# Kernel optimization log

Measured on AMD Instinct MI355X. Metric: run time of the kernel, lower is better.

Reference implementation:

```python
import jax, jax.numpy as jnp
import numpy as np

N = 50000      # nodes
E = 800000     # edges (avg degree 16)
DIN = 128
HID = 128
OUT = 10       # classes
G = 64         # graphs in batch


def setup_inputs() -> dict:
    key = jax.random.key(0)
    ks = jax.random.split(key, 10)
    x = jax.random.normal(ks[0], (N, DIN), dtype=jnp.float32)
    edge_index = jax.random.randint(ks[1], (2, E), 0, N, dtype=jnp.int32)
    edge_weight = jax.random.uniform(ks[2], (E,), dtype=jnp.float32)
    batch = jnp.sort(jax.random.randint(ks[3], (N,), 0, G, dtype=jnp.int32))
    W1 = jax.random.normal(ks[4], (DIN, HID), dtype=jnp.float32) / np.sqrt(DIN)
    b1 = jnp.zeros((HID,), dtype=jnp.float32)
    W2 = jax.random.normal(ks[5], (HID, HID), dtype=jnp.float32) / np.sqrt(HID)
    b2 = jnp.zeros((HID,), dtype=jnp.float32)
    W3 = jax.random.normal(ks[6], (HID, OUT), dtype=jnp.float32) / np.sqrt(HID)
    b3 = jnp.zeros((OUT,), dtype=jnp.float32)
    return {"x": x, "edge_index": edge_index, "edge_weight": edge_weight,
            "batch": batch, "W1": W1, "b1": b1, "W2": W2, "b2": b2,
            "W3": W3, "b3": b3}


def _gcn_norm(edge_index, edge_weight, n_nodes):
    # PyG gcn_norm: add self-loops with weight 1, D^-1/2 (A+I) D^-1/2
    loop = jnp.arange(n_nodes, dtype=edge_index.dtype)
    src = jnp.concatenate([edge_index[0], loop])
    dst = jnp.concatenate([edge_index[1], loop])
    w = jnp.concatenate([edge_weight, jnp.ones((n_nodes,), edge_weight.dtype)])
    deg = jax.ops.segment_sum(w, dst, num_segments=n_nodes)
    dinv = jnp.where(deg > 0, jax.lax.rsqrt(deg), 0.0)
    norm = dinv[src] * w * dinv[dst]
    return src, dst, norm


def _gcn_conv(x, W, b, src, dst, norm, n_nodes):
    h = x @ W                                      # [N, F] dense transform
    msg = norm[:, None] * h[src]                   # gather + scale  [E+N, F]
    out = jax.ops.segment_sum(msg, dst, num_segments=n_nodes)  # scatter-add
    return out + b


def reference(x, edge_index, edge_weight, batch, W1, b1, W2, b2, W3, b3):
    src, dst, norm = _gcn_norm(edge_index, edge_weight, N)
    h = jax.nn.relu(_gcn_conv(x, W1, b1, src, dst, norm, N))
    h = jax.nn.relu(_gcn_conv(h, W2, b2, src, dst, norm, N))
    h = _gcn_conv(h, W3, b3, src, dst, norm, N)    # [N, OUT]
    # global_mean_pool over graph ids
    sums = jax.ops.segment_sum(h, batch, num_segments=G)          # [G, OUT]
    cnts = jax.ops.segment_sum(jnp.ones((N,), h.dtype), batch, num_segments=G)
    pooled = sums / jnp.maximum(cnts, 1.0)[:, None]
    return jax.nn.log_softmax(pooled, axis=1)
```

## Files before the change

kernel.cpp:

```cpp
#include <hip/hip_runtime.h>
#include <math.h>

#define NN 50000
#define EE 800000
#define GG 64
#define FD 128
#define OUTD 10
#define NB 49

typedef __attribute__((ext_vector_type(8))) short s8v;
typedef __attribute__((ext_vector_type(4))) float f4v;

static __device__ inline unsigned short f2b(float f) {
    unsigned int u = __float_as_uint(f);
    return (unsigned short)((u + 0x7FFFu + ((u >> 16) & 1u)) >> 16);
}

#define DEG_SCALE 4294967296.0
#define DEG_MASK  ((1ull << 44) - 1)


__global__ void k_prep(unsigned long long* packed, const float* __restrict__ W1,
                       const float* __restrict__ W2, unsigned short* __restrict__ Wt1,
                       unsigned short* __restrict__ Wt2, int n) {
    int i = blockIdx.x * blockDim.x + threadIdx.x;
    if (i < n) packed[i] = (1ull << 44) | (1ull << 32);
    if (i < FD * FD) {
        int nn = i >> 7, k = i & 127;
        Wt1[i] = f2b(W1[k * FD + nn]);
        Wt2[i] = f2b(W2[k * FD + nn]);
    }
}

__global__ void k_degree(const int* __restrict__ dst, const float* __restrict__ w,
                         unsigned long long* packed, unsigned* __restrict__ rank, int e) {
    int i = blockIdx.x * blockDim.x + threadIdx.x;
    if (i >= e) return;
    unsigned long long q = (unsigned long long)((double)w[i] * DEG_SCALE + 0.5);
    unsigned long long old = atomicAdd(&packed[dst[i]], (1ull << 44) | q);
    rank[i] = (unsigned)(old >> 44) - 1u;
}

__global__ __launch_bounds__(1024) void k_scanA(const unsigned long long* __restrict__ packed,
        int* __restrict__ rowptr, int* __restrict__ blocksum,
        float* __restrict__ dinv, int n) {
    __shared__ int wtot[16];
    int tid = threadIdx.x;
    int i = blockIdx.x * 1024 + tid;
    int lane = tid & 63, wv = tid >> 6;
    int v = 0;
    if (i < n) {
        unsigned long long p = packed[i];
        v = (int)(p >> 44);
        float deg = (float)((double)(p & DEG_MASK) * (1.0 / DEG_SCALE));
        dinv[i] = 1.0f / sqrtf(deg);
    }
    int s = v;
    #pragma unroll
    for (int off = 1; off < 64; off <<= 1) {
        int u = __shfl_up(s, off, 64);
        if (lane >= off) s += u;
    }
    if (lane == 63) wtot[wv] = s;
    __syncthreads();
    int wpre = 0;
    for (int j = 0; j < wv; ++j) wpre += wtot[j];
    if (i < n) rowptr[i] = wpre + s - v;
    if (tid == 1023) blocksum[blockIdx.x] = wpre + s;
}

__global__ void k_scanB(int* blocksum, int* rowptr) {
    int l = threadIdx.x;
    int v = (l < NB) ? blocksum[l] : 0;
    int s = v;
    #pragma unroll
    for (int off = 1; off < 64; off <<= 1) {
        int u = __shfl_up(s, off, 64);
        if (l >= off) s += u;
    }
    if (l < NB) blocksum[l] = s - v;
    if (l == NB - 1) rowptr[NN] = s;
}

__global__ __launch_bounds__(1024) void k_scanC(int* __restrict__ rowptr,
        const int* __restrict__ blocksum, const unsigned long long* __restrict__ packed,
        const float* __restrict__ dinv, uint2* __restrict__ ent, int n) {
    int i = blockIdx.x * 1024 + threadIdx.x;
    if (i >= n) return;
    int r = rowptr[i] + blocksum[blockIdx.x];
    rowptr[i] = r;
    int cnt = (int)(packed[i] >> 44);
    float di = dinv[i];
    ent[r + cnt - 1] = make_uint2((unsigned)i, __float_as_uint(di * di));
}

__global__ void k_fill(const int* __restrict__ src, const int* __restrict__ dst,
                       const float* __restrict__ w, const float* __restrict__ dinv,
                       const int* __restrict__ rowptr, const unsigned* __restrict__ rank,
                       uint2* __restrict__ ent, int e) {
    int i = blockIdx.x * blockDim.x + threadIdx.x;
    if (i >= e) return;
    int s = src[i], d = dst[i];
    int pos = rowptr[d] + (int)rank[i];
    float v = dinv[s] * w[i] * dinv[d];
    ent[pos] = make_uint2((unsigned)s, __float_as_uint(v));
}

__global__ void k_bounds(const int* __restrict__ batch, int* __restrict__ gstart, int n) {
    int i = blockIdx.x * blockDim.x + threadIdx.x;
    if (i >= n) return;
    int b = batch[i];
    int bp = (i == 0) ? -1 : batch[i - 1];
    for (int g = bp + 1; g <= b; ++g) gstart[g] = i;
    if (i == n - 1)
        for (int g = b + 1; g <= GG; ++g) gstart[g] = n;
}

__global__ __launch_bounds__(256) void k_gemm_f32in(const float* __restrict__ A,
        const unsigned short* __restrict__ Wt, unsigned short* __restrict__ out, int n) {
    int tid = threadIdx.x;
    int wave = tid >> 6, lane = tid & 63;
    int quad = lane >> 4, c16 = lane & 15;
    int rowbase = blockIdx.x * 64 + wave * 16;
    int rowA = rowbase + c16;
    if (rowA >= n) rowA = n - 1;
    f4v acc[8];
    #pragma unroll
    for (int t = 0; t < 8; ++t) acc[t] = (f4v){0.f, 0.f, 0.f, 0.f};

    #pragma unroll
    for (int k0 = 0; k0 < 128; k0 += 32) {
        const float* ap = A + (size_t)rowA * FD + k0 + quad * 8;
        float4 a0 = *(const float4*)ap;
        float4 a1 = *(const float4*)(ap + 4);
        s8v a;
        a[0] = (short)f2b(a0.x); a[1] = (short)f2b(a0.y);
        a[2] = (short)f2b(a0.z); a[3] = (short)f2b(a0.w);
        a[4] = (short)f2b(a1.x); a[5] = (short)f2b(a1.y);
        a[6] = (short)f2b(a1.z); a[7] = (short)f2b(a1.w);
        #pragma unroll
        for (int t = 0; t < 8; ++t) {
            s8v b = *(const s8v*)(Wt + (size_t)(t * 16 + c16) * FD + k0 + quad * 8);
            acc[t] = __builtin_amdgcn_mfma_f32_16x16x32_bf16(a, b, acc[t], 0, 0, 0);
        }
    }
    #pragma unroll
    for (int t = 0; t < 8; ++t) {
        #pragma unroll
        for (int r = 0; r < 4; ++r) {
            int row = rowbase + quad * 4 + r;
            if (row < n) out[(size_t)row * FD + t * 16 + c16] = f2b(acc[t][r]);
        }
    }
}

__global__ __launch_bounds__(256) void k_gemm_bf(const unsigned short* __restrict__ A,
        const unsigned short* __restrict__ Wt, unsigned short* __restrict__ out, int n) {
    int tid = threadIdx.x;
    int wave = tid >> 6, lane = tid & 63;
    int quad = lane >> 4, c16 = lane & 15;
    int rowbase = blockIdx.x * 64 + wave * 16;
    int rowA = rowbase + c16;
    if (rowA >= n) rowA = n - 1;
    f4v acc[8];
    #pragma unroll
    for (int t = 0; t < 8; ++t) acc[t] = (f4v){0.f, 0.f, 0.f, 0.f};

    #pragma unroll
    for (int k0 = 0; k0 < 128; k0 += 32) {
        s8v a = *(const s8v*)(A + (size_t)rowA * FD + k0 + quad * 8);
        #pragma unroll
        for (int t = 0; t < 8; ++t) {
            s8v b = *(const s8v*)(Wt + (size_t)(t * 16 + c16) * FD + k0 + quad * 8);
            acc[t] = __builtin_amdgcn_mfma_f32_16x16x32_bf16(a, b, acc[t], 0, 0, 0);
        }
    }
    #pragma unroll
    for (int t = 0; t < 8; ++t) {
        #pragma unroll
        for (int r = 0; r < 4; ++r) {
            int row = rowbase + quad * 4 + r;
            if (row < n) out[(size_t)row * FD + t * 16 + c16] = f2b(acc[t][r]);
        }
    }
}

__global__ void k_gemm10(const unsigned short* __restrict__ A, const float* __restrict__ W,
                         float* __restrict__ out, int n) {
    __shared__ float Ws[FD * OUTD];
    int tid = threadIdx.x;
    for (int i = tid; i < FD * OUTD; i += blockDim.x) Ws[i] = W[i];
    __syncthreads();
    int i = blockIdx.x * blockDim.x + tid;
    if (i >= n) return;
    float acc[OUTD];
    #pragma unroll
    for (int c = 0; c < OUTD; ++c) acc[c] = 0.0f;
    const unsigned short* a = A + (size_t)i * FD;
    for (int k0 = 0; k0 < FD; k0 += 8) {
        uint4 t = *(const uint4*)(a + k0);
        float av[8];
        av[0] = __uint_as_float(t.x << 16); av[1] = __uint_as_float(t.x & 0xFFFF0000u);
        av[2] = __uint_as_float(t.y << 16); av[3] = __uint_as_float(t.y & 0xFFFF0000u);
        av[4] = __uint_as_float(t.z << 16); av[5] = __uint_as_float(t.z & 0xFFFF0000u);
        av[6] = __uint_as_float(t.w << 16); av[7] = __uint_as_float(t.w & 0xFFFF0000u);
        #pragma unroll
        for (int j = 0; j < 8; ++j)
            #pragma unroll
            for (int c = 0; c < OUTD; ++c) acc[c] += av[j] * Ws[(k0 + j) * OUTD + c];
    }
    float* o = out + (size_t)i * OUTD;
    #pragma unroll
    for (int c = 0; c < OUTD; ++c) o[c] = acc[c];
}

__global__ __launch_bounds__(256) void k_spmm_bf(const int* __restrict__ rowptr,
        const uint2* __restrict__ ent, const unsigned short* __restrict__ tin,
        const float* __restrict__ bias, unsigned short* __restrict__ out,
        int n, int dorelu) {
    int w = (blockIdx.x * blockDim.x + threadIdx.x) >> 6;
    int lane = threadIdx.x & 63;
    if (w >= n) return;
    int c = lane & 15, g = lane >> 4;
    int beg = rowptr[w], end = rowptr[w + 1];
    float acc[8];
    #pragma unroll
    for (int j = 0; j < 8; ++j) acc[j] = 0.0f;
    for (int e0 = beg; e0 < end; e0 += 16) {
        uint2 en[4];
        uint4 t[4];
        #pragma unroll
        for (int u = 0; u < 4; ++u) {
            int e = e0 + 4 * u + g;
            en[u] = (e < end) ? ent[e] : make_uint2(0u, 0u);
        }
        #pragma unroll
        for (int u = 0; u < 4; ++u)
            t[u] = *(const uint4*)(tin + (size_t)en[u].x * FD + c * 8);
        #pragma unroll
        for (int u = 0; u < 4; ++u) {
            float v = __uint_as_float(en[u].y);
            acc[0] += v * __uint_as_float(t[u].x << 16);
            acc[1] += v * __uint_as_float(t[u].x & 0xFFFF0000u);
            acc[2] += v * __uint_as_float(t[u].y << 16);
            acc[3] += v * __uint_as_float(t[u].y & 0xFFFF0000u);
            acc[4] += v * __uint_as_float(t[u].z << 16);
            acc[5] += v * __uint_as_float(t[u].z & 0xFFFF0000u);
            acc[6] += v * __uint_as_float(t[u].w << 16);
            acc[7] += v * __uint_as_float(t[u].w & 0xFFFF0000u);
        }
    }
    #pragma unroll
    for (int j = 0; j < 8; ++j) {
        acc[j] += __shfl_xor(acc[j], 16, 64);
        acc[j] += __shfl_xor(acc[j], 32, 64);
    }
    if (g == 0) {
        uint4 r;
        float o[8];
        #pragma unroll
        for (int j = 0; j < 8; ++j) {
            float x = acc[j] + bias[c * 8 + j];
            o[j] = dorelu ? fmaxf(x, 0.0f) : x;
        }
        r.x = (unsigned)f2b(o[0]) | ((unsigned)f2b(o[1]) << 16);
        r.y = (unsigned)f2b(o[2]) | ((unsigned)f2b(o[3]) << 16);
        r.z = (unsigned)f2b(o[4]) | ((unsigned)f2b(o[5]) << 16);
        r.w = (unsigned)f2b(o[6]) | ((unsigned)f2b(o[7]) << 16);
        *(uint4*)(out + (size_t)w * FD + c * 8) = r;
    }
}

__global__ void k_spmm10(const int* __restrict__ rowptr, const uint2* __restrict__ ent,
        const float* __restrict__ tin, const float* __restrict__ bias,
        float* __restrict__ out, int n) {
    int t = blockIdx.x * blockDim.x + threadIdx.x;
    int node = t / OUTD;
    int c = t - node * OUTD;
    if (node >= n) return;
    int beg = rowptr[node], end = rowptr[node + 1];
    float acc = 0.0f;
    for (int e = beg; e < end; ++e) {
        uint2 en = ent[e];
        acc += __uint_as_float(en.y) * tin[(size_t)en.x * OUTD + c];
    }
    out[(size_t)node * OUTD + c] = acc + bias[c];
}


__global__ __launch_bounds__(256) void k_poolfin(const float* __restrict__ h,
        const int* __restrict__ gstart, float* __restrict__ out) {
    int g = blockIdx.x;
    int beg = gstart[g], end = gstart[g + 1];
    int tid = threadIdx.x;
    int lane = tid & 63, wv = tid >> 6;
    float acc[OUTD];
    #pragma unroll
    for (int c = 0; c < OUTD; ++c) acc[c] = 0.0f;
    for (int i = beg + tid; i < end; i += 256) {
        const float* hp = h + (size_t)i * OUTD;
        #pragma unroll
        for (int c = 0; c < OUTD; ++c) acc[c] += hp[c];
    }
    #pragma unroll
    for (int off = 32; off >= 1; off >>= 1)
        #pragma unroll
        for (int c = 0; c < OUTD; ++c) acc[c] += __shfl_down(acc[c], off, 64);
    __shared__ float ws[4][OUTD];
    if (lane == 0)
        #pragma unroll
        for (int c = 0; c < OUTD; ++c) ws[wv][c] = acc[c];
    __syncthreads();
    if (tid == 0) {
        float cf = fmaxf((float)(end - beg), 1.0f);
        float v[OUTD], m = -1e30f;
        #pragma unroll
        for (int c = 0; c < OUTD; ++c) {
            v[c] = (ws[0][c] + ws[1][c] + ws[2][c] + ws[3][c]) / cf;
            m = fmaxf(m, v[c]);
        }
        float s = 0.0f;
        #pragma unroll
        for (int c = 0; c < OUTD; ++c) s += expf(v[c] - m);
        float l = logf(s);
        #pragma unroll
        for (int c = 0; c < OUTD; ++c) out[g * OUTD + c] = v[c] - m - l;
    }
}


extern "C" void kernel_launch(void* const* d_in, const int* in_sizes, int n_in,
                              void* d_out, int out_size, void* d_ws, size_t ws_size,
                              hipStream_t stream) {
    const float* x   = (const float*)d_in[0];
    const int*   ei  = (const int*)d_in[1];
    const float* ew  = (const float*)d_in[2];
    const int*   bat = (const int*)d_in[3];
    const float* W1  = (const float*)d_in[4];
    const float* b1  = (const float*)d_in[5];
    const float* W2  = (const float*)d_in[6];
    const float* b2  = (const float*)d_in[7];
    const float* W3  = (const float*)d_in[8];
    const float* b3  = (const float*)d_in[9];
    float* out = (float*)d_out;

    const int* src = ei;
    const int* dst = ei + EE;

    char* p = (char*)d_ws;
    auto alloc = [&](size_t bytes) -> void* {
        void* r = (void*)p;
        p += (bytes + 255) & ~(size_t)255;
        return r;
    };
    unsigned long long* packed = (unsigned long long*)alloc((size_t)NN * 8);
    float*          dinv   = (float*)alloc((size_t)NN * 4);
    int*            rowptr = (int*)  alloc((size_t)(NN + 1) * 4);
    unsigned*       rank   = (unsigned*)alloc((size_t)EE * 4);
    uint2*          ent    = (uint2*)alloc((size_t)(EE + NN) * 8);
    unsigned short* Wt1    = (unsigned short*)alloc((size_t)FD * FD * 2);
    unsigned short* Wt2    = (unsigned short*)alloc((size_t)FD * FD * 2);
    unsigned short* hA     = (unsigned short*)alloc((size_t)NN * FD * 2);
    unsigned short* hB     = (unsigned short*)alloc((size_t)NN * FD * 2);
    float*          bufC   = (float*)alloc((size_t)NN * OUTD * 4);
    float*          bufD   = (float*)alloc((size_t)NN * OUTD * 4);
    int*            bsum   = (int*)  alloc((size_t)(NB + 1) * 4);
    int*            gstart = (int*)  alloc((size_t)(GG + 1) * 4);
    (void)ws_size; (void)in_sizes; (void)n_in; (void)out_size;

    const int B = 256;
    k_prep  <<<(NN + B - 1) / B, B, 0, stream>>>(packed, W1, W2, Wt1, Wt2, NN);
    k_degree<<<(EE + B - 1) / B, B, 0, stream>>>(dst, ew, packed, rank, EE);
    k_scanA <<<NB, 1024, 0, stream>>>(packed, rowptr, bsum, dinv, NN);
    k_scanB <<<1, 64, 0, stream>>>(bsum, rowptr);
    k_scanC <<<NB, 1024, 0, stream>>>(rowptr, bsum, packed, dinv, ent, NN);
    k_fill  <<<(EE + B - 1) / B, B, 0, stream>>>(src, dst, ew, dinv, rowptr, rank, ent, EE);
    k_bounds<<<(NN + B - 1) / B, B, 0, stream>>>(bat, gstart, NN);

    k_gemm_f32in<<<(NN + 63) / 64, B, 0, stream>>>(x, Wt1, hA, NN);
    k_spmm_bf   <<<(NN * 64 + B - 1) / B, B, 0, stream>>>(rowptr, ent, hA, b1, hB, NN, 1);
    k_gemm_bf   <<<(NN + 63) / 64, B, 0, stream>>>(hB, Wt2, hA, NN);
    k_spmm_bf   <<<(NN * 64 + B - 1) / B, B, 0, stream>>>(rowptr, ent, hA, b2, hB, NN, 1);
    k_gemm10    <<<(NN + B - 1) / B, B, 0, stream>>>(hB, W3, bufC, NN);
    k_spmm10    <<<(NN * OUTD + B - 1) / B, B, 0, stream>>>(rowptr, ent, bufC, b3, bufD, NN);
    k_poolfin   <<<GG, 256, 0, stream>>>(bufD, gstart, out);
}
```

Baseline: 297.3 us.

## Merge preprocessing kernels and use single-pass decoupled scan

Fuses the first GEMM, the degree/rank atomics and the graph-bound computation into one heterogeneous launch partitioned by block index, so independent work shares one grid. Replaces the three-kernel scan (scanA/scanB/scanC) with a single kernel where each block publishes its sum and spins on flags of earlier blocks to get its base offset. This removes several launches and inter-kernel gaps. It relies on all 49 scan blocks being co-resident for the spin-wait to be safe.

```diff
diff --git a/kernel.cpp b/kernel.cpp
--- a/kernel.cpp
+++ b/kernel.cpp
@@ -7,6 +7,9 @@
 #define FD 128
 #define OUTD 10
 #define NB 49
+#define GB 782
+#define DB 3125
+#define BB 196
 
 typedef __attribute__((ext_vector_type(8))) short s8v;
 typedef __attribute__((ext_vector_type(4))) float f4v;
@@ -22,7 +25,7 @@
 
 __global__ void k_prep(unsigned long long* packed, const float* __restrict__ W1,
                        const float* __restrict__ W2, unsigned short* __restrict__ Wt1,
-                       unsigned short* __restrict__ Wt2, int n) {
+                       unsigned short* __restrict__ Wt2, int* __restrict__ bflag, int n) {
     int i = blockIdx.x * blockDim.x + threadIdx.x;
     if (i < n) packed[i] = (1ull << 44) | (1ull << 32);
     if (i < FD * FD) {
@@ -30,30 +33,93 @@
         Wt1[i] = f2b(W1[k * FD + nn]);
         Wt2[i] = f2b(W2[k * FD + nn]);
     }
-}
-
-__global__ void k_degree(const int* __restrict__ dst, const float* __restrict__ w,
-                         unsigned long long* packed, unsigned* __restrict__ rank, int e) {
-    int i = blockIdx.x * blockDim.x + threadIdx.x;
-    if (i >= e) return;
-    unsigned long long q = (unsigned long long)((double)w[i] * DEG_SCALE + 0.5);
-    unsigned long long old = atomicAdd(&packed[dst[i]], (1ull << 44) | q);
-    rank[i] = (unsigned)(old >> 44) - 1u;
-}
-
-__global__ __launch_bounds__(1024) void k_scanA(const unsigned long long* __restrict__ packed,
-        int* __restrict__ rowptr, int* __restrict__ blocksum,
-        float* __restrict__ dinv, int n) {
+    if (i < NB) bflag[i] = 0;
+}
+
+
+static __device__ inline void gemm_f32in_body(int bid, const float* __restrict__ A,
+        const unsigned short* __restrict__ Wt, unsigned short* __restrict__ out, int n) {
+    int tid = threadIdx.x;
+    int wave = tid >> 6, lane = tid & 63;
+    int quad = lane >> 4, c16 = lane & 15;
+    int rowbase = bid * 64 + wave * 16;
+    int rowA = rowbase + c16;
+    if (rowA >= n) rowA = n - 1;
+    f4v acc[8];
+    #pragma unroll
+    for (int t = 0; t < 8; ++t) acc[t] = (f4v){0.f, 0.f, 0.f, 0.f};
+    #pragma unroll
+    for (int k0 = 0; k0 < 128; k0 += 32) {
+        const float* ap = A + (size_t)rowA * FD + k0 + quad * 8;
+        float4 a0 = *(const float4*)ap;
+        float4 a1 = *(const float4*)(ap + 4);
+        s8v a;
+        a[0] = (short)f2b(a0.x); a[1] = (short)f2b(a0.y);
+        a[2] = (short)f2b(a0.z); a[3] = (short)f2b(a0.w);
+        a[4] = (short)f2b(a1.x); a[5] = (short)f2b(a1.y);
+        a[6] = (short)f2b(a1.z); a[7] = (short)f2b(a1.w);
+        #pragma unroll
+        for (int t = 0; t < 8; ++t) {
+            s8v b = *(const s8v*)(Wt + (size_t)(t * 16 + c16) * FD + k0 + quad * 8);
+            acc[t] = __builtin_amdgcn_mfma_f32_16x16x32_bf16(a, b, acc[t], 0, 0, 0);
+        }
+    }
+    #pragma unroll
+    for (int t = 0; t < 8; ++t) {
+        #pragma unroll
+        for (int r = 0; r < 4; ++r) {
+            int row = rowbase + quad * 4 + r;
+            if (row < n) out[(size_t)row * FD + t * 16 + c16] = f2b(acc[t][r]);
+        }
+    }
+}
+
+__global__ __launch_bounds__(256) void k_mega1(const float* __restrict__ x,
+        const unsigned short* __restrict__ Wt1, unsigned short* __restrict__ hA,
+        const int* __restrict__ dst, const float* __restrict__ ew,
+        unsigned long long* packed, unsigned* __restrict__ rank,
+        const int* __restrict__ batch, int* __restrict__ gstart) {
+    int b = blockIdx.x;
+    if (b < GB) {
+        gemm_f32in_body(b, x, Wt1, hA, NN);
+    } else if (b < GB + DB) {
+        int i = (b - GB) * 256 + threadIdx.x;
+        if (i < EE) {
+            unsigned long long q = (unsigned long long)((double)ew[i] * DEG_SCALE + 0.5);
+            unsigned long long old = atomicAdd(&packed[dst[i]], (1ull << 44) | q);
+            rank[i] = (unsigned)(old >> 44) - 1u;
+        }
+    } else {
+        int i = (b - GB - DB) * 256 + threadIdx.x;
+        if (i < NN) {
+            int bb = batch[i];
+            int bp = (i == 0) ? -1 : batch[i - 1];
+            for (int g = bp + 1; g <= bb; ++g) gstart[g] = i;
+            if (i == NN - 1)
+                for (int g = bb + 1; g <= GG; ++g) gstart[g] = NN;
+        }
+    }
+}
+
+
+__global__ __launch_bounds__(1024) void k_scan(const unsigned long long* __restrict__ packed,
+        int* __restrict__ rowptr, float* __restrict__ dinv, uint2* __restrict__ ent,
+        int* __restrict__ bsum, int* __restrict__ bflag, int n) {
     __shared__ int wtot[16];
+    __shared__ int sbase_sh;
     int tid = threadIdx.x;
-    int i = blockIdx.x * 1024 + tid;
+    int bid = blockIdx.x;
+    int i = bid * 1024 + tid;
     int lane = tid & 63, wv = tid >> 6;
+
     int v = 0;
+    float di = 0.0f;
     if (i < n) {
         unsigned long long p = packed[i];
         v = (int)(p >> 44);
         float deg = (float)((double)(p & DEG_MASK) * (1.0 / DEG_SCALE));
-        dinv[i] = 1.0f / sqrtf(deg);
+        di = 1.0f / sqrtf(deg);
+        dinv[i] = di;
     }
     int s = v;
     #pragma unroll
@@ -63,35 +129,36 @@
     }
     if (lane == 63) wtot[wv] = s;
     __syncthreads();
+
+    int btot = 0;
+    #pragma unroll
+    for (int j = 0; j < 16; ++j) btot += wtot[j];
+    if (tid == 0) {
+        bsum[bid] = btot;
+        __hip_atomic_store(&bflag[bid], 1, __ATOMIC_RELEASE, __HIP_MEMORY_SCOPE_AGENT);
+    }
+    if (tid < 64) {
+        int acc = 0;
+        if (tid < bid) {
+            while (__hip_atomic_load(&bflag[tid], __ATOMIC_ACQUIRE,
+                                     __HIP_MEMORY_SCOPE_AGENT) == 0) {}
+            acc = bsum[tid];
+        }
+        #pragma unroll
+        for (int off = 32; off >= 1; off >>= 1) acc += __shfl_xor(acc, off, 64);
+        if (tid == 0) sbase_sh = acc;
+    }
+    __syncthreads();
+    int base = sbase_sh;
+
     int wpre = 0;
     for (int j = 0; j < wv; ++j) wpre += wtot[j];
-    if (i < n) rowptr[i] = wpre + s - v;
-    if (tid == 1023) blocksum[blockIdx.x] = wpre + s;
-}
-
-__global__ void k_scanB(int* blocksum, int* rowptr) {
-    int l = threadIdx.x;
-    int v = (l < NB) ? blocksum[l] : 0;
-    int s = v;
-    #pragma unroll
-    for (int off = 1; off < 64; off <<= 1) {
-        int u = __shfl_up(s, off, 64);
-        if (l >= off) s += u;
-    }
-    if (l < NB) blocksum[l] = s - v;
-    if (l == NB - 1) rowptr[NN] = s;
-}
-
-__global__ __launch_bounds__(1024) void k_scanC(int* __restrict__ rowptr,
-        const int* __restrict__ blocksum, const unsigned long long* __restrict__ packed,
-        const float* __restrict__ dinv, uint2* __restrict__ ent, int n) {
-    int i = blockIdx.x * 1024 + threadIdx.x;
-    if (i >= n) return;
-    int r = rowptr[i] + blocksum[blockIdx.x];
-    rowptr[i] = r;
-    int cnt = (int)(packed[i] >> 44);
-    float di = dinv[i];
-    ent[r + cnt - 1] = make_uint2((unsigned)i, __float_as_uint(di * di));
+    if (i < n) {
+        int r = base + wpre + (s - v);
+        rowptr[i] = r;
+        ent[r + v - 1] = make_uint2((unsigned)i, __float_as_uint(di * di));
+    }
+    if (bid == NB - 1 && tid == 0) rowptr[n] = base + btot;
 }
 
 __global__ void k_fill(const int* __restrict__ src, const int* __restrict__ dst,
@@ -106,53 +173,6 @@
     ent[pos] = make_uint2((unsigned)s, __float_as_uint(v));
 }
 
-__global__ void k_bounds(const int* __restrict__ batch, int* __restrict__ gstart, int n) {
-    int i = blockIdx.x * blockDim.x + threadIdx.x;
-    if (i >= n) return;
-    int b = batch[i];
-    int bp = (i == 0) ? -1 : batch[i - 1];
-    for (int g = bp + 1; g <= b; ++g) gstart[g] = i;
-    if (i == n - 1)
-        for (int g = b + 1; g <= GG; ++g) gstart[g] = n;
-}
-
-__global__ __launch_bounds__(256) void k_gemm_f32in(const float* __restrict__ A,
-        const unsigned short* __restrict__ Wt, unsigned short* __restrict__ out, int n) {
-    int tid = threadIdx.x;
-    int wave = tid >> 6, lane = tid & 63;
-    int quad = lane >> 4, c16 = lane & 15;
-    int rowbase = blockIdx.x * 64 + wave * 16;
-    int rowA = rowbase + c16;
-    if (rowA >= n) rowA = n - 1;
-    f4v acc[8];
-    #pragma unroll
-    for (int t = 0; t < 8; ++t) acc[t] = (f4v){0.f, 0.f, 0.f, 0.f};
-
-    #pragma unroll
-    for (int k0 = 0; k0 < 128; k0 += 32) {
-        const float* ap = A + (size_t)rowA * FD + k0 + quad * 8;
-        float4 a0 = *(const float4*)ap;
-        float4 a1 = *(const float4*)(ap + 4);
-        s8v a;
-        a[0] = (short)f2b(a0.x); a[1] = (short)f2b(a0.y);
-        a[2] = (short)f2b(a0.z); a[3] = (short)f2b(a0.w);
-        a[4] = (short)f2b(a1.x); a[5] = (short)f2b(a1.y);
-        a[6] = (short)f2b(a1.z); a[7] = (short)f2b(a1.w);
-        #pragma unroll
-        for (int t = 0; t < 8; ++t) {
-            s8v b = *(const s8v*)(Wt + (size_t)(t * 16 + c16) * FD + k0 + quad * 8);
-            acc[t] = __builtin_amdgcn_mfma_f32_16x16x32_bf16(a, b, acc[t], 0, 0, 0);
-        }
-    }
-    #pragma unroll
-    for (int t = 0; t < 8; ++t) {
-        #pragma unroll
-        for (int r = 0; r < 4; ++r) {
-            int row = rowbase + quad * 4 + r;
-            if (row < n) out[(size_t)row * FD + t * 16 + c16] = f2b(acc[t][r]);
-        }
-    }
-}
 
 __global__ __launch_bounds__(256) void k_gemm_bf(const unsigned short* __restrict__ A,
         const unsigned short* __restrict__ Wt, unsigned short* __restrict__ out, int n) {
@@ -165,7 +185,6 @@
     f4v acc[8];
     #pragma unroll
     for (int t = 0; t < 8; ++t) acc[t] = (f4v){0.f, 0.f, 0.f, 0.f};
-
     #pragma unroll
     for (int k0 = 0; k0 < 128; k0 += 32) {
         s8v a = *(const s8v*)(A + (size_t)rowA * FD + k0 + quad * 8);
@@ -364,24 +383,21 @@
     unsigned short* hB     = (unsigned short*)alloc((size_t)NN * FD * 2);
     float*          bufC   = (float*)alloc((size_t)NN * OUTD * 4);
     float*          bufD   = (float*)alloc((size_t)NN * OUTD * 4);
-    int*            bsum   = (int*)  alloc((size_t)(NB + 1) * 4);
+    int*            bsum   = (int*)  alloc((size_t)NB * 4);
+    int*            bflag  = (int*)  alloc((size_t)NB * 4);
     int*            gstart = (int*)  alloc((size_t)(GG + 1) * 4);
     (void)ws_size; (void)in_sizes; (void)n_in; (void)out_size;
 
     const int B = 256;
-    k_prep  <<<(NN + B - 1) / B, B, 0, stream>>>(packed, W1, W2, Wt1, Wt2, NN);
-    k_degree<<<(EE + B - 1) / B, B, 0, stream>>>(dst, ew, packed, rank, EE);
-    k_scanA <<<NB, 1024, 0, stream>>>(packed, rowptr, bsum, dinv, NN);
-    k_scanB <<<1, 64, 0, stream>>>(bsum, rowptr);
-    k_scanC <<<NB, 1024, 0, stream>>>(rowptr, bsum, packed, dinv, ent, NN);
-    k_fill  <<<(EE + B - 1) / B, B, 0, stream>>>(src, dst, ew, dinv, rowptr, rank, ent, EE);
-    k_bounds<<<(NN + B - 1) / B, B, 0, stream>>>(bat, gstart, NN);
-
-    k_gemm_f32in<<<(NN + 63) / 64, B, 0, stream>>>(x, Wt1, hA, NN);
-    k_spmm_bf   <<<(NN * 64 + B - 1) / B, B, 0, stream>>>(rowptr, ent, hA, b1, hB, NN, 1);
-    k_gemm_bf   <<<(NN + 63) / 64, B, 0, stream>>>(hB, Wt2, hA, NN);
-    k_spmm_bf   <<<(NN * 64 + B - 1) / B, B, 0, stream>>>(rowptr, ent, hA, b2, hB, NN, 1);
-    k_gemm10    <<<(NN + B - 1) / B, B, 0, stream>>>(hB, W3, bufC, NN);
-    k_spmm10    <<<(NN * OUTD + B - 1) / B, B, 0, stream>>>(rowptr, ent, bufC, b3, bufD, NN);
-    k_poolfin   <<<GG, 256, 0, stream>>>(bufD, gstart, out);
-}
+    k_prep <<<(NN + B - 1) / B, B, 0, stream>>>(packed, W1, W2, Wt1, Wt2, bflag, NN);
+    k_mega1<<<GB + DB + BB, B, 0, stream>>>(x, Wt1, hA, dst, ew, packed, rank, bat, gstart);
+    k_scan <<<NB, 1024, 0, stream>>>(packed, rowptr, dinv, ent, bsum, bflag, NN);
+    k_fill <<<(EE + B - 1) / B, B, 0, stream>>>(src, dst, ew, dinv, rowptr, rank, ent, EE);
+
+    k_spmm_bf<<<(NN * 64 + B - 1) / B, B, 0, stream>>>(rowptr, ent, hA, b1, hB, NN, 1);
+    k_gemm_bf<<<GB, B, 0, stream>>>(hB, Wt2, hA, NN);
+    k_spmm_bf<<<(NN * 64 + B - 1) / B, B, 0, stream>>>(rowptr, ent, hA, b2, hB, NN, 1);
+    k_gemm10 <<<(NN + B - 1) / B, B, 0, stream>>>(hB, W3, bufC, NN);
+    k_spmm10 <<<(NN * OUTD + B - 1) / B, B, 0, stream>>>(rowptr, ent, bufC, b3, bufD, NN);
+    k_poolfin<<<GG, 256, 0, stream>>>(bufD, gstart, out);
+}
```

After: 282.4 us. 5.0% less time.
